# Kernel optimization log

Hardware: AMD Instinct MI355X
Metric: run time of the kernel (lower is better)

## Reference

```python
import jax, jax.numpy as jnp
import numpy as np

NEG_SLOPE = 0.2  # PyG GATConv default leaky_relu slope
EPS = 1e-16     # PyG softmax denominator epsilon


def gat_conv(x, src, dst, W, att_src, att_dst, bias, concat, num_nodes):
    """PyG-style GATConv (eval mode, dropout disabled).
    x: [N, F_in]; W: [F_in, H*C]; att_src/att_dst: [H, C]; bias: [H*C] or [C].
    Messages flow src -> dst; softmax is per destination node."""
    H, C = att_src.shape
    h = (x @ W).reshape(num_nodes, H, C)                      # [N,H,C]
    a_src = jnp.sum(h * att_src[None], axis=-1)               # [N,H]
    a_dst = jnp.sum(h * att_dst[None], axis=-1)               # [N,H]
    e = jax.nn.leaky_relu(a_src[src] + a_dst[dst], NEG_SLOPE) # [E,H]
    # numerically-stable segment softmax over edges grouped by dst
    m = jax.ops.segment_max(e, dst, num_segments=num_nodes)   # [N,H]
    ex = jnp.exp(e - m[dst])                                  # [E,H]
    s = jax.ops.segment_sum(ex, dst, num_segments=num_nodes)  # [N,H]
    alpha = ex / (s[dst] + EPS)                               # [E,H]
    msg = h[src] * alpha[..., None]                           # [E,H,C]
    out = jax.ops.segment_sum(msg, dst, num_segments=num_nodes)  # [N,H,C]
    if concat:
        out = out.reshape(num_nodes, H * C)
    else:
        out = out.mean(axis=1)                                # [N,C]
    return out + bias, alpha


def setup_inputs() -> dict:
    key = jax.random.key(0)
    ks = jax.random.split(key, 20)
    N, E = 50000, 500000
    F_node = 128       # num_node_features
    SED = 128          # sentence_embedding_dim
    HID = 64           # hidden_channels
    H = 2              # num_heads

    def g(k, shape, scale=0.05):
        return jax.random.normal(k, shape, dtype=jnp.float32) * scale

    return {
        "x": jax.random.normal(ks[0], (N, SED), dtype=jnp.float32),
        "edge_index": jax.random.randint(ks[1], (2, E), 0, N, dtype=jnp.int64),
        "cls_emb": jax.random.normal(ks[2], (768,), dtype=jnp.float32),
        # fc0: Linear(768, SED)
        "fc0_w": g(ks[3], (SED, 768)), "fc0_b": g(ks[4], (SED,)),
        # conv1: GATConv(2*SED -> HID, heads=H, concat=True)
        "W1": g(ks[5], (2 * SED, H * HID)),
        "att_src1": g(ks[6], (H, HID)), "att_dst1": g(ks[7], (H, HID)),
        "bias1": g(ks[8], (H * HID,)),
        # conv2: GATConv(H*HID -> F_node, heads=H, concat=False)
        "W2": g(ks[9], (H * HID, H * F_node)),
        "att_src2": g(ks[10], (H, F_node)), "att_dst2": g(ks[11], (H, F_node)),
        "bias2": g(ks[12], (F_node,)),
        # edge MLP head
        "fc2_w": g(ks[13], (F_node, 2 * F_node)), "fc2_b": g(ks[14], (F_node,)),
        "fc3_w": g(ks[15], (1, F_node)), "fc3_b": g(ks[16], (1,)),
    }


def reference(x, edge_index, cls_emb, fc0_w, fc0_b,
              W1, att_src1, att_dst1, bias1,
              W2, att_src2, att_dst2, bias2,
              fc2_w, fc2_b, fc3_w, fc3_b):
    N = x.shape[0]
    src, dst = edge_index[0], edge_index[1]
    # sentence embedding projection + broadcast-concat to every node
    sent = fc0_w @ cls_emb + fc0_b                                # [SED]
    h = jnp.concatenate([x, jnp.broadcast_to(sent, (N, sent.shape[0]))], axis=1)
    h, _ = gat_conv(h, src, dst, W1, att_src1, att_dst1, bias1, True, N)
    h = jax.nn.elu(h)
    h, _ = gat_conv(h, src, dst, W2, att_src2, att_dst2, bias2, False, N)
    # edge head: gather endpoints, concat, MLP, sigmoid
    edge_input = jnp.concatenate([h[src], h[dst]], axis=1)        # [E, 2*F]
    z = jax.nn.relu(edge_input @ fc2_w.T + fc2_b)                 # [E, F]
    logits = z @ fc3_w.T + fc3_b                                  # [E, 1]
    return jax.nn.sigmoid(logits)
```

## Files before the change

### kernel.cpp

```cpp
#include <hip/hip_runtime.h>
#include <hip/hip_bf16.h>
#include <math.h>


typedef short short8 __attribute__((ext_vector_type(8)));
typedef float floatx4 __attribute__((ext_vector_type(4)));
typedef float v2f __attribute__((ext_vector_type(2)));
typedef unsigned uint2v __attribute__((ext_vector_type(2)));

__device__ __forceinline__ v2f bfpair(unsigned v) {
    uint2v t; t.x = v << 16; t.y = v & 0xFFFF0000u;
    return __builtin_bit_cast(v2f, t);
}
__device__ __forceinline__ unsigned short bfbits(float f) {
    return __builtin_bit_cast(unsigned short, __float2bfloat16(f));
}
__device__ __forceinline__ unsigned packbf(float a, float b) {
    return ((unsigned)bfbits(b) << 16) | (unsigned)bfbits(a);
}
__device__ __forceinline__ float lrelu(float v) { return v > 0.f ? v : 0.2f * v; }

__global__ void prep_kernel(const float* __restrict__ cls, const float* __restrict__ fc0_w,
                            const float* __restrict__ fc0_b, const float* __restrict__ W1,
                            const float* __restrict__ W2, const float* __restrict__ fc2_w,
                            float* __restrict__ c1,
                            __hip_bfloat16* __restrict__ w1frag,
                            __hip_bfloat16* __restrict__ w2frag,
                            __hip_bfloat16* __restrict__ fc2frag,
                            int* __restrict__ counts, int N) {
    int tid = threadIdx.x;
    int gstride = gridDim.x * blockDim.x;
    int g = blockIdx.x * blockDim.x + tid;
    for (int i = g; i < N; i += gstride) counts[i] = 0;
    if (blockIdx.x == 0) {
        __shared__ float s_sent[128];
        if (tid < 128) {
            float acc = fc0_b[tid];
            const float* row = fc0_w + (size_t)tid * 768;
            for (int k = 0; k < 768; ++k) acc += row[k] * cls[k];
            s_sent[tid] = acc;
        }
        __syncthreads();
        if (tid < 128) {
            float acc = 0.f;
            for (int k = 0; k < 128; ++k) acc += s_sent[k] * W1[(128 + k) * 128 + tid];
            c1[tid] = acc;
        }
    }
    for (int i = g; i < 16384; i += gstride) {
        int j = i & 7, l = (i >> 3) & 63, nt = (i >> 9) & 7, kt = (i >> 12) & 3;
        int k = kt * 32 + (l >> 4) * 8 + j;
        int n = nt * 16 + (l & 15);
        w1frag[i] = __float2bfloat16(W1[k * 128 + n]);
    }
    for (int i = g; i < 32768; i += gstride) {
        int j = i & 7, l = (i >> 3) & 63, nt = (i >> 9) & 15, kt = (i >> 13) & 3;
        int k = kt * 32 + (l >> 4) * 8 + j;
        int n = nt * 16 + (l & 15);
        w2frag[i] = __float2bfloat16(W2[k * 256 + n]);
    }
    for (int i = g; i < 32768; i += gstride) {
        int j = i & 7, l = (i >> 3) & 63, nt = (i >> 9) & 15, kt = (i >> 13) & 3;
        int k = kt * 32 + (l >> 4) * 8 + j;
        int n = nt * 16 + (l & 15);
        float v = (n < 128) ? fc2_w[n * 256 + k] : fc2_w[(n - 128) * 256 + 128 + k];
        fc2frag[i] = __float2bfloat16(v);
    }
}

__global__ void __launch_bounds__(256) bsum_kernel(const int* __restrict__ counts,
                                                   int* __restrict__ bsum, int N) {
    int base = blockIdx.x * 1024;
    int tid = threadIdx.x;
    int v = 0;
    #pragma unroll
    for (int k = 0; k < 4; ++k) {
        int idx = base + k * 256 + tid;
        if (idx < N) v += counts[idx];
    }
    #pragma unroll
    for (int off = 1; off < 64; off <<= 1) v += __shfl_xor(v, off, 64);
    __shared__ int ws[4];
    if ((tid & 63) == 0) ws[tid >> 6] = v;
    __syncthreads();
    if (tid == 0) bsum[blockIdx.x] = ws[0] + ws[1] + ws[2] + ws[3];
}

__global__ void top_scan_kernel(const int* __restrict__ bsum, int* __restrict__ boff, int nb) {
    int lane = threadIdx.x;
    int v = (lane < nb) ? bsum[lane] : 0;
    int x = v;
    #pragma unroll
    for (int off = 1; off < 64; off <<= 1) {
        int t = __shfl_up(x, off, 64);
        if (lane >= off) x += t;
    }
    if (lane < nb) boff[lane] = x - v;
}

__global__ void __launch_bounds__(1024) local_scan_kernel(const int* __restrict__ counts,
                                                          const int* __restrict__ boff,
                                                          int* __restrict__ row, int* __restrict__ woff,
                                                          int N, int E) {
    int tid = threadIdx.x, lane = tid & 63, wv = tid >> 6;
    int base = blockIdx.x * 1024;
    __shared__ int wsum[16];
    int v = (base + tid < N) ? counts[base + tid] : 0;
    int x = v;
    #pragma unroll
    for (int off = 1; off < 64; off <<= 1) {
        int t = __shfl_up(x, off, 64);
        if (lane >= off) x += t;
    }
    if (lane == 63) wsum[wv] = x;
    __syncthreads();
    if (wv == 0 && lane < 16) {
        int y = wsum[lane];
        #pragma unroll
        for (int off = 1; off < 16; off <<= 1) {
            int t = __shfl_up(y, off, 64);
            if (lane >= off) y += t;
        }
        wsum[lane] = y;
    }
    __syncthreads();
    int excl = boff[blockIdx.x] + (wv ? wsum[wv - 1] : 0) + x - v;
    if (base + tid < N) { row[base + tid] = excl; woff[base + tid] = excl; }
    if (blockIdx.x == 0 && tid == 0) row[N] = E;
}

__global__ void scatter_kernel(const int* __restrict__ src, const int* __restrict__ dst,
                               int* __restrict__ woff, int* __restrict__ srcs, int E) {
    int e = blockIdx.x * blockDim.x + threadIdx.x;
    if (e < E) {
        int pos = atomicAdd(&woff[dst[e]], 1);
        srcs[pos] = src[e];
    }
}

__global__ void __launch_bounds__(256) gemm1_count_kernel(
        const float* __restrict__ x, const __hip_bfloat16* __restrict__ wfrag,
        const float* __restrict__ c1, const float* __restrict__ att_s, const float* __restrict__ att_d,
        __hip_bfloat16* __restrict__ h1bf, float* __restrict__ a_src, float* __restrict__ a_dst,
        const int* __restrict__ dst, int* __restrict__ counts, int E, int G1, int N) {
    if ((int)blockIdx.x >= G1) {
        int e = ((int)blockIdx.x - G1) * 256 + threadIdx.x;
        if (e < E) atomicAdd(&counts[dst[e]], 1);
        return;
    }
    int lane = threadIdx.x & 63, wv = threadIdx.x >> 6;
    int lo = lane & 15, quad = lane >> 4;
    int rowbase = ((int)blockIdx.x * 4 + wv) * 16;
    if (rowbase >= N) return;
    int arow = rowbase + lo; if (arow >= N) arow = N - 1;
    const float* ap = x + (size_t)arow * 128 + quad * 8;
    floatx4 acc[8];
    #pragma unroll
    for (int nt = 0; nt < 8; ++nt) acc[nt] = (floatx4){0.f, 0.f, 0.f, 0.f};
    const short8* bf = (const short8*)wfrag;
    #pragma unroll
    for (int kt = 0; kt < 4; ++kt) {
        float4 fa = *(const float4*)(ap + kt * 32);
        float4 fb = *(const float4*)(ap + kt * 32 + 4);
        short8 a;
        a[0] = (short)bfbits(fa.x); a[1] = (short)bfbits(fa.y);
        a[2] = (short)bfbits(fa.z); a[3] = (short)bfbits(fa.w);
        a[4] = (short)bfbits(fb.x); a[5] = (short)bfbits(fb.y);
        a[6] = (short)bfbits(fb.z); a[7] = (short)bfbits(fb.w);
        #pragma unroll
        for (int nt = 0; nt < 8; ++nt)
            acc[nt] = __builtin_amdgcn_mfma_f32_16x16x32_bf16(a, bf[(kt * 8 + nt) * 64 + lane], acc[nt], 0, 0, 0);
    }
    float ps0[4] = {0,0,0,0}, ps1[4] = {0,0,0,0}, pd0[4] = {0,0,0,0}, pd1[4] = {0,0,0,0};
    #pragma unroll
    for (int nt = 0; nt < 8; ++nt) {
        int ch = nt * 16 + lo;
        float cv = c1[ch], as_v = att_s[ch], ad_v = att_d[ch];
        #pragma unroll
        for (int r = 0; r < 4; ++r) {
            int row = rowbase + quad * 4 + r;
            float val = acc[nt][r] + cv;
            if (row < N) ((unsigned short*)h1bf)[(size_t)row * 128 + ch] = bfbits(val);
            if (nt < 4) { ps0[r] += val * as_v; pd0[r] += val * ad_v; }
            else        { ps1[r] += val * as_v; pd1[r] += val * ad_v; }
        }
    }
    #pragma unroll
    for (int r = 0; r < 4; ++r) {
        int row = rowbase + quad * 4 + r;
        float v0 = ps0[r], v1 = ps1[r], v2 = pd0[r], v3 = pd1[r];
        #pragma unroll
        for (int off = 1; off < 16; off <<= 1) {
            v0 += __shfl_xor(v0, off, 64); v1 += __shfl_xor(v1, off, 64);
            v2 += __shfl_xor(v2, off, 64); v3 += __shfl_xor(v3, off, 64);
        }
        if (lo == 0 && row < N) {
            a_src[row * 2 + 0] = v0; a_src[row * 2 + 1] = v1;
            a_dst[row * 2 + 0] = v2; a_dst[row * 2 + 1] = v3;
        }
    }
}

__global__ void __launch_bounds__(256) agg1_csr_kernel(
        const int* __restrict__ row, const int* __restrict__ srcs,
        const float* __restrict__ a_src, const float* __restrict__ a_dst,
        const unsigned* __restrict__ h1u, const float* __restrict__ bias1,
        unsigned* __restrict__ hmid_u, int N) {
    int tid = threadIdx.x;
    int d = blockIdx.x * 16 + (tid >> 4);
    if (d >= N) return;
    int q = tid & 15;
    int beg = row[d], end = row[d + 1];
    float2 adp = ((const float2*)a_dst)[d];
    float den0 = 0.f, den1 = 0.f;
    v2f facc2[4];
    #pragma unroll
    for (int m = 0; m < 4; ++m) facc2[m] = (v2f){0.f, 0.f};
    for (int i = beg; i < end; i += 4) {
        bool h1 = (i + 1) < end, h2 = (i + 2) < end, h3 = (i + 3) < end;
        int s0 = srcs[i];
        int s1 = h1 ? srcs[i + 1] : s0;
        int s2 = h2 ? srcs[i + 2] : s0;
        int s3 = h3 ? srcs[i + 3] : s0;
        float2 as0 = ((const float2*)a_src)[s0];
        float2 as1 = ((const float2*)a_src)[s1];
        float2 as2 = ((const float2*)a_src)[s2];
        float2 as3 = ((const float2*)a_src)[s3];
        uint4 u0 = ((const uint4*)(h1u + (size_t)s0 * 64))[q];
        uint4 u1 = ((const uint4*)(h1u + (size_t)s1 * 64))[q];
        uint4 u2 = ((const uint4*)(h1u + (size_t)s2 * 64))[q];
        uint4 u3 = ((const uint4*)(h1u + (size_t)s3 * 64))[q];
        float e00 = __expf(lrelu(as0.x + adp.x));
        float e01 = __expf(lrelu(as0.y + adp.y));
        float e10 = h1 ? __expf(lrelu(as1.x + adp.x)) : 0.f;
        float e11 = h1 ? __expf(lrelu(as1.y + adp.y)) : 0.f;
        float e20 = h2 ? __expf(lrelu(as2.x + adp.x)) : 0.f;
        float e21 = h2 ? __expf(lrelu(as2.y + adp.y)) : 0.f;
        float e30 = h3 ? __expf(lrelu(as3.x + adp.x)) : 0.f;
        float e31 = h3 ? __expf(lrelu(as3.y + adp.y)) : 0.f;
        den0 += e00 + e10 + e20 + e30;
        den1 += e01 + e11 + e21 + e31;
        float w0 = (q < 8) ? e00 : e01;
        float w1 = (q < 8) ? e10 : e11;
        float w2 = (q < 8) ? e20 : e21;
        float w3 = (q < 8) ? e30 : e31;
        facc2[0] += bfpair(u0.x) * w0 + bfpair(u1.x) * w1 + bfpair(u2.x) * w2 + bfpair(u3.x) * w3;
        facc2[1] += bfpair(u0.y) * w0 + bfpair(u1.y) * w1 + bfpair(u2.y) * w2 + bfpair(u3.y) * w3;
        facc2[2] += bfpair(u0.z) * w0 + bfpair(u1.z) * w1 + bfpair(u2.z) * w2 + bfpair(u3.z) * w3;
        facc2[3] += bfpair(u0.w) * w0 + bfpair(u1.w) * w1 + bfpair(u2.w) * w2 + bfpair(u3.w) * w3;
    }
    float inv = 1.f / (((q < 8) ? den0 : den1) + 1e-16f);
    int c0 = 8 * q;
    float v[8];
    #pragma unroll
    for (int m = 0; m < 4; ++m) {
        float va = facc2[m].x * inv + bias1[c0 + 2 * m];
        float vb = facc2[m].y * inv + bias1[c0 + 2 * m + 1];
        v[2 * m]     = va > 0.f ? va : expm1f(va);
        v[2 * m + 1] = vb > 0.f ? vb : expm1f(vb);
    }
    uint4 o;
    o.x = packbf(v[0], v[1]); o.y = packbf(v[2], v[3]);
    o.z = packbf(v[4], v[5]); o.w = packbf(v[6], v[7]);
    ((uint4*)(hmid_u + (size_t)d * 64))[q] = o;
}

__global__ void __launch_bounds__(256) gemm2_mfma_kernel(
        const __hip_bfloat16* __restrict__ hmid, const __hip_bfloat16* __restrict__ wfrag,
        const float* __restrict__ att_s, const float* __restrict__ att_d,
        __hip_bfloat16* __restrict__ h2pre, float* __restrict__ a_src, float* __restrict__ a_dst, int N) {
    int lane = threadIdx.x & 63, wv = threadIdx.x >> 6;
    int lo = lane & 15, quad = lane >> 4;
    int rowbase = (blockIdx.x * 4 + wv) * 16;
    if (rowbase >= N) return;
    int arow = rowbase + lo; if (arow >= N) arow = N - 1;
    const __hip_bfloat16* ap = hmid + (size_t)arow * 128 + quad * 8;
    floatx4 acc[16];
    #pragma unroll
    for (int nt = 0; nt < 16; ++nt) acc[nt] = (floatx4){0.f, 0.f, 0.f, 0.f};
    const short8* bf = (const short8*)wfrag;
    #pragma unroll
    for (int kt = 0; kt < 4; ++kt) {
        short8 a = *(const short8*)(ap + kt * 32);
        #pragma unroll
        for (int nt = 0; nt < 16; ++nt)
            acc[nt] = __builtin_amdgcn_mfma_f32_16x16x32_bf16(a, bf[(kt * 16 + nt) * 64 + lane], acc[nt], 0, 0, 0);
    }
    float ps0[4] = {0,0,0,0}, ps1[4] = {0,0,0,0}, pd0[4] = {0,0,0,0}, pd1[4] = {0,0,0,0};
    #pragma unroll
    for (int nt = 0; nt < 16; ++nt) {
        int ch = nt * 16 + lo;
        float as_v = att_s[ch], ad_v = att_d[ch];
        #pragma unroll
        for (int r = 0; r < 4; ++r) {
            int row = rowbase + quad * 4 + r;
            float val = acc[nt][r];
            if (row < N) ((unsigned short*)h2pre)[(size_t)row * 256 + ch] = bfbits(val);
            if (nt < 8) { ps0[r] += val * as_v; pd0[r] += val * ad_v; }
            else        { ps1[r] += val * as_v; pd1[r] += val * ad_v; }
        }
    }
    #pragma unroll
    for (int r = 0; r < 4; ++r) {
        int row = rowbase + quad * 4 + r;
        float v0 = ps0[r], v1 = ps1[r], v2 = pd0[r], v3 = pd1[r];
        #pragma unroll
        for (int off = 1; off < 16; off <<= 1) {
            v0 += __shfl_xor(v0, off, 64); v1 += __shfl_xor(v1, off, 64);
            v2 += __shfl_xor(v2, off, 64); v3 += __shfl_xor(v3, off, 64);
        }
        if (lo == 0 && row < N) {
            a_src[row * 2 + 0] = v0; a_src[row * 2 + 1] = v1;
            a_dst[row * 2 + 0] = v2; a_dst[row * 2 + 1] = v3;
        }
    }
}

__global__ void __launch_bounds__(256) agg2_csr_kernel(
        const int* __restrict__ row, const int* __restrict__ srcs,
        const float* __restrict__ a_src, const float* __restrict__ a_dst,
        const unsigned* __restrict__ h2u, const float* __restrict__ bias2,
        unsigned* __restrict__ h2bf_u, int N) {
    int tid = threadIdx.x;
    int d = blockIdx.x * 8 + (tid >> 5);
    if (d >= N) return;
    int q = tid & 31;
    int beg = row[d], end = row[d + 1];
    float2 adp = ((const float2*)a_dst)[d];
    float den0 = 0.f, den1 = 0.f;
    v2f facc2[4];
    #pragma unroll
    for (int m = 0; m < 4; ++m) facc2[m] = (v2f){0.f, 0.f};
    for (int i = beg; i < end; i += 4) {
        bool h1 = (i + 1) < end, h2 = (i + 2) < end, h3 = (i + 3) < end;
        int s0 = srcs[i];
        int s1 = h1 ? srcs[i + 1] : s0;
        int s2 = h2 ? srcs[i + 2] : s0;
        int s3 = h3 ? srcs[i + 3] : s0;
        float2 as0 = ((const float2*)a_src)[s0];
        float2 as1 = ((const float2*)a_src)[s1];
        float2 as2 = ((const float2*)a_src)[s2];
        float2 as3 = ((const float2*)a_src)[s3];
        uint4 u0 = ((const uint4*)(h2u + (size_t)s0 * 128))[q];
        uint4 u1 = ((const uint4*)(h2u + (size_t)s1 * 128))[q];
        uint4 u2 = ((const uint4*)(h2u + (size_t)s2 * 128))[q];
        uint4 u3 = ((const uint4*)(h2u + (size_t)s3 * 128))[q];
        float e00 = __expf(lrelu(as0.x + adp.x));
        float e01 = __expf(lrelu(as0.y + adp.y));
        float e10 = h1 ? __expf(lrelu(as1.x + adp.x)) : 0.f;
        float e11 = h1 ? __expf(lrelu(as1.y + adp.y)) : 0.f;
        float e20 = h2 ? __expf(lrelu(as2.x + adp.x)) : 0.f;
        float e21 = h2 ? __expf(lrelu(as2.y + adp.y)) : 0.f;
        float e30 = h3 ? __expf(lrelu(as3.x + adp.x)) : 0.f;
        float e31 = h3 ? __expf(lrelu(as3.y + adp.y)) : 0.f;
        den0 += e00 + e10 + e20 + e30;
        den1 += e01 + e11 + e21 + e31;
        float w0 = (q < 16) ? e00 : e01;
        float w1 = (q < 16) ? e10 : e11;
        float w2 = (q < 16) ? e20 : e21;
        float w3 = (q < 16) ? e30 : e31;
        facc2[0] += bfpair(u0.x) * w0 + bfpair(u1.x) * w1 + bfpair(u2.x) * w2 + bfpair(u3.x) * w3;
        facc2[1] += bfpair(u0.y) * w0 + bfpair(u1.y) * w1 + bfpair(u2.y) * w2 + bfpair(u3.y) * w3;
        facc2[2] += bfpair(u0.z) * w0 + bfpair(u1.z) * w1 + bfpair(u2.z) * w2 + bfpair(u3.z) * w3;
        facc2[3] += bfpair(u0.w) * w0 + bfpair(u1.w) * w1 + bfpair(u2.w) * w2 + bfpair(u3.w) * w3;
    }
    float inv = 0.5f / (((q < 16) ? den0 : den1) + 1e-16f);
    #pragma unroll
    for (int m = 0; m < 4; ++m) {
        facc2[m] *= inv;
        facc2[m].x += __shfl_xor(facc2[m].x, 16, 64);
        facc2[m].y += __shfl_xor(facc2[m].y, 16, 64);
    }
    if (q < 16) {
        int c0 = 8 * q;
        uint4 o;
        o.x = packbf(facc2[0].x + bias2[c0 + 0], facc2[0].y + bias2[c0 + 1]);
        o.y = packbf(facc2[1].x + bias2[c0 + 2], facc2[1].y + bias2[c0 + 3]);
        o.z = packbf(facc2[2].x + bias2[c0 + 4], facc2[2].y + bias2[c0 + 5]);
        o.w = packbf(facc2[3].x + bias2[c0 + 6], facc2[3].y + bias2[c0 + 7]);
        ((uint4*)(h2bf_u + (size_t)d * 64))[q] = o;
    }
}

__global__ void __launch_bounds__(256) zsd_mfma_kernel(
        const __hip_bfloat16* __restrict__ h2bf, const __hip_bfloat16* __restrict__ wfrag,
        const float* __restrict__ fc2_b, __hip_bfloat16* __restrict__ zsd, int N) {
    int lane = threadIdx.x & 63, wv = threadIdx.x >> 6;
    int lo = lane & 15, quad = lane >> 4;
    int rowbase = (blockIdx.x * 4 + wv) * 16;
    if (rowbase >= N) return;
    int arow = rowbase + lo; if (arow >= N) arow = N - 1;
    const __hip_bfloat16* ap = h2bf + (size_t)arow * 128 + quad * 8;
    floatx4 acc[16];
    #pragma unroll
    for (int nt = 0; nt < 16; ++nt) acc[nt] = (floatx4){0.f, 0.f, 0.f, 0.f};
    const short8* bf = (const short8*)wfrag;
    #pragma unroll
    for (int kt = 0; kt < 4; ++kt) {
        short8 a = *(const short8*)(ap + kt * 32);
        #pragma unroll
        for (int nt = 0; nt < 16; ++nt)
            acc[nt] = __builtin_amdgcn_mfma_f32_16x16x32_bf16(a, bf[(kt * 16 + nt) * 64 + lane], acc[nt], 0, 0, 0);
    }
    #pragma unroll
    for (int nt = 0; nt < 16; ++nt) {
        int ch = nt * 16 + lo;
        float bv = (nt >= 8) ? fc2_b[ch - 128] : 0.f;
        #pragma unroll
        for (int r = 0; r < 4; ++r) {
            int row = rowbase + quad * 4 + r;
            if (row < N) ((unsigned short*)zsd)[(size_t)row * 256 + ch] = bfbits(acc[nt][r] + bv);
        }
    }
}

__global__ void __launch_bounds__(256) edge_zsd_kernel(
        const int* __restrict__ src, const int* __restrict__ dst,
        const unsigned* __restrict__ zsd_u, const float* __restrict__ fc3_w,
        const float* __restrict__ fc3_b, float* __restrict__ out, int E) {
    int lane = threadIdx.x & 63, wv = threadIdx.x >> 6;
    int g = lane >> 5, r = (lane >> 4) & 1, q = lane & 15;
    int base = (blockIdx.x * 4 + wv) * 16;
    if (base >= E) return;
    v2f f30 = {fc3_w[8 * q + 4 * r + 0], fc3_w[8 * q + 4 * r + 1]};
    v2f f31 = {fc3_w[8 * q + 4 * r + 2], fc3_w[8 * q + 4 * r + 3]};
    float b3 = fc3_b[0];
    int nodes[8];
    #pragma unroll
    for (int j = 0; j < 8; ++j) {
        int e = base + 2 * j + g;
        int ec = e < E ? e : E - 1;
        nodes[j] = r ? dst[ec] : src[ec];
    }
    uint4 rows[8];
    #pragma unroll
    for (int j = 0; j < 8; ++j)
        rows[j] = ((const uint4*)(zsd_u + (size_t)nodes[j] * 128 + (r << 6)))[q];
    #pragma unroll
    for (int j = 0; j < 8; ++j) {
        uint4 mine = rows[j];
        unsigned sx = (unsigned)__shfl_xor((int)mine.x, 16, 64);
        unsigned sy = (unsigned)__shfl_xor((int)mine.y, 16, 64);
        unsigned sz = (unsigned)__shfl_xor((int)mine.z, 16, 64);
        unsigned sw = (unsigned)__shfl_xor((int)mine.w, 16, 64);
        unsigned mA = r ? mine.z : mine.x;
        unsigned mB = r ? mine.w : mine.y;
        unsigned oA = r ? sz : sx;
        unsigned oB = r ? sw : sy;
        v2f sA = bfpair(mA) + bfpair(oA);
        v2f sB = bfpair(mB) + bfpair(oB);
        sA.x = fmaxf(sA.x, 0.f); sA.y = fmaxf(sA.y, 0.f);
        sB.x = fmaxf(sB.x, 0.f); sB.y = fmaxf(sB.y, 0.f);
        v2f p2 = sA * f30 + sB * f31;
        float p = p2.x + p2.y;
        #pragma unroll
        for (int off = 1; off < 32; off <<= 1) p += __shfl_xor(p, off, 64);
        int e = base + 2 * j + g;
        if ((lane & 31) == 0 && e < E)
            out[e] = 1.f / (1.f + expf(-(p + b3)));
    }
}

extern "C" void kernel_launch(void* const* d_in, const int* in_sizes, int n_in,
                              void* d_out, int out_size, void* d_ws, size_t ws_size,
                              hipStream_t stream) {
    const float* x      = (const float*)d_in[0];
    const int*   ei     = (const int*)d_in[1];
    const float* cls    = (const float*)d_in[2];
    const float* fc0_w  = (const float*)d_in[3];
    const float* fc0_b  = (const float*)d_in[4];
    const float* W1     = (const float*)d_in[5];
    const float* att_s1 = (const float*)d_in[6];
    const float* att_d1 = (const float*)d_in[7];
    const float* bias1  = (const float*)d_in[8];
    const float* W2     = (const float*)d_in[9];
    const float* att_s2 = (const float*)d_in[10];
    const float* att_d2 = (const float*)d_in[11];
    const float* bias2  = (const float*)d_in[12];
    const float* fc2_w  = (const float*)d_in[13];
    const float* fc2_b  = (const float*)d_in[14];
    const float* fc3_w  = (const float*)d_in[15];
    const float* fc3_b  = (const float*)d_in[16];
    float* out = (float*)d_out;

    int N = in_sizes[0] / 128;
    int E = in_sizes[1] / 2;
    const int* src = ei;
    const int* dst = ei + E;
    int nb = (N + 1023) / 1024;

    float* w = (float*)d_ws;
    size_t off = 0;
    auto alloc = [&](size_t n) { float* p = w + off; off += (n + 63) & ~(size_t)63; return p; };
    float* c1      = alloc(128);
    float* w1fragf = alloc(16384 / 2);
    float* w2fragf = alloc(32768 / 2);
    float* fc2fragf= alloc(32768 / 2);
    float* a_s1    = alloc((size_t)N * 2);
    float* a_d1    = alloc((size_t)N * 2);
    float* a_s2    = alloc((size_t)N * 2);
    float* a_d2    = alloc((size_t)N * 2);
    float* h1bff   = alloc((size_t)N * 64);
    float* hmidf   = alloc((size_t)N * 64);
    float* h2pref  = alloc((size_t)N * 128);
    float* h2bff   = alloc((size_t)N * 64);
    float* zsdf    = alloc((size_t)N * 128);
    int* counts = (int*)alloc(N);
    int* rowp   = (int*)alloc(N + 1);
    int* woff   = (int*)alloc(N);
    int* srcs   = (int*)alloc(E);
    int* bsum   = (int*)alloc(64);
    int* boff   = (int*)alloc(64);
    __hip_bfloat16* w1frag = (__hip_bfloat16*)w1fragf;
    __hip_bfloat16* w2frag = (__hip_bfloat16*)w2fragf;
    __hip_bfloat16* fc2frag= (__hip_bfloat16*)fc2fragf;
    __hip_bfloat16* hmid   = (__hip_bfloat16*)hmidf;
    __hip_bfloat16* h2pre  = (__hip_bfloat16*)h2pref;
    __hip_bfloat16* h2bf   = (__hip_bfloat16*)h2bff;
    __hip_bfloat16* h1bf   = (__hip_bfloat16*)h1bff;
    __hip_bfloat16* zsd    = (__hip_bfloat16*)zsdf;

    prep_kernel<<<64, 256, 0, stream>>>(cls, fc0_w, fc0_b, W1, W2, fc2_w, c1, w1frag, w2frag, fc2frag,
                                        counts, N);
    int G1 = (N + 63) / 64;
    int G2 = (E + 255) / 256;
    gemm1_count_kernel<<<G1 + G2, 256, 0, stream>>>(x, w1frag, c1, att_s1, att_d1, h1bf, a_s1, a_d1,
                                                    dst, counts, E, G1, N);
    bsum_kernel<<<nb, 256, 0, stream>>>(counts, bsum, N);
    top_scan_kernel<<<1, 64, 0, stream>>>(bsum, boff, nb);
    local_scan_kernel<<<nb, 1024, 0, stream>>>(counts, boff, rowp, woff, N, E);
    scatter_kernel<<<(E + 255) / 256, 256, 0, stream>>>(src, dst, woff, srcs, E);
    agg1_csr_kernel<<<(N + 15) / 16, 256, 0, stream>>>(rowp, srcs, a_s1, a_d1, (const unsigned*)h1bf, bias1, (unsigned*)hmid, N);
    gemm2_mfma_kernel<<<(N + 63) / 64, 256, 0, stream>>>(hmid, w2frag, att_s2, att_d2, h2pre, a_s2, a_d2, N);
    agg2_csr_kernel<<<(N + 7) / 8, 256, 0, stream>>>(rowp, srcs, a_s2, a_d2, (const unsigned*)h2pre, bias2, (unsigned*)h2bf, N);
    zsd_mfma_kernel<<<(N + 63) / 64, 256, 0, stream>>>(h2bf, fc2frag, fc2_b, zsd, N);
    edge_zsd_kernel<<<(E + 63) / 64, 256, 0, stream>>>(src, dst, (const unsigned*)zsd, fc3_w, fc3_b, out, E);
}
```

Before: 329.4 us.

## Fold W2 into fc2 weights and aggregate layer-2 on 128-wide hmid

Uses linearity to reorder layer 2: the aggregation runs over the 128-channel hmid features per head instead of the 256-channel projected h2, and W2 is pre-multiplied into fc2 (with the head mean) as one 256x256 weight. The second-layer attention scores are computed in agg1's epilogue via precomputed W2·att vectors, which removes the gemm2 kernel and the h2pre round trip. The aggregation gather now reads half the bytes per edge. In exchange the zsd GEMM's K doubles to 256, and prep does a serial 128-length dot per weight element, about 65k of them.

```diff
diff --git a/kernel.cpp b/kernel.cpp
--- a/kernel.cpp
+++ b/kernel.cpp
@@ -23,10 +23,13 @@
 __global__ void prep_kernel(const float* __restrict__ cls, const float* __restrict__ fc0_w,
                             const float* __restrict__ fc0_b, const float* __restrict__ W1,
                             const float* __restrict__ W2, const float* __restrict__ fc2_w,
+                            const float* __restrict__ fc2_b, const float* __restrict__ bias2,
+                            const float* __restrict__ att_s2, const float* __restrict__ att_d2,
                             float* __restrict__ c1,
                             __hip_bfloat16* __restrict__ w1frag,
-                            __hip_bfloat16* __restrict__ w2frag,
-                            __hip_bfloat16* __restrict__ fc2frag,
+                            __hip_bfloat16* __restrict__ wbigfrag,
+                            float* __restrict__ v2s, float* __restrict__ v2d,
+                            float* __restrict__ bz,
                             int* __restrict__ counts, int N) {
     int tid = threadIdx.x;
     int gstride = gridDim.x * blockDim.x;
@@ -53,18 +56,34 @@
         int n = nt * 16 + (l & 15);
         w1frag[i] = __float2bfloat16(W1[k * 128 + n]);
     }
-    for (int i = g; i < 32768; i += gstride) {
-        int j = i & 7, l = (i >> 3) & 63, nt = (i >> 9) & 15, kt = (i >> 13) & 3;
+    for (int i = g; i < 65536; i += gstride) {
+        int j = i & 7, l = (i >> 3) & 63, nt = (i >> 9) & 15, kt = (i >> 13) & 7;
         int k = kt * 32 + (l >> 4) * 8 + j;
         int n = nt * 16 + (l & 15);
-        w2frag[i] = __float2bfloat16(W2[k * 256 + n]);
-    }
-    for (int i = g; i < 32768; i += gstride) {
-        int j = i & 7, l = (i >> 3) & 63, nt = (i >> 9) & 15, kt = (i >> 13) & 3;
-        int k = kt * 32 + (l >> 4) * 8 + j;
-        int n = nt * 16 + (l & 15);
-        float v = (n < 128) ? fc2_w[n * 256 + k] : fc2_w[(n - 128) * 256 + 128 + k];
-        fc2frag[i] = __float2bfloat16(v);
+        int h = k >> 7, kp = k & 127;
+        const float* w2row = W2 + (size_t)kp * 256 + h * 128;
+        const float* fcrow = (n < 128) ? (fc2_w + (size_t)n * 256)
+                                       : (fc2_w + (size_t)(n - 128) * 256 + 128);
+        float acc = 0.f;
+        for (int c2 = 0; c2 < 128; ++c2) acc += w2row[c2] * fcrow[c2];
+        wbigfrag[i] = __float2bfloat16(0.5f * acc);
+    }
+    for (int i = g; i < 256; i += gstride) {
+        int h = i >> 7, kp = i & 127;
+        const float* w2row = W2 + (size_t)kp * 256 + h * 128;
+        const float* as = att_s2 + h * 128;
+        const float* ad = att_d2 + h * 128;
+        float s = 0.f, dd = 0.f;
+        for (int c = 0; c < 128; ++c) { s += w2row[c] * as[c]; dd += w2row[c] * ad[c]; }
+        v2s[i] = s; v2d[i] = dd;
+    }
+    for (int i = g; i < 256; i += gstride) {
+        const float* fcrow = (i < 128) ? (fc2_w + (size_t)i * 256)
+                                       : (fc2_w + (size_t)(i - 128) * 256 + 128);
+        float acc = 0.f;
+        for (int c = 0; c < 128; ++c) acc += bias2[c] * fcrow[c];
+        if (i >= 128) acc += fc2_b[i - 128];
+        bz[i] = acc;
     }
 }
 
@@ -205,7 +224,8 @@
         const int* __restrict__ row, const int* __restrict__ srcs,
         const float* __restrict__ a_src, const float* __restrict__ a_dst,
         const unsigned* __restrict__ h1u, const float* __restrict__ bias1,
-        unsigned* __restrict__ hmid_u, int N) {
+        const float* __restrict__ v2s, const float* __restrict__ v2d,
+        unsigned* __restrict__ hmid_u, float* __restrict__ a_s2, float* __restrict__ a_d2, int N) {
     int tid = threadIdx.x;
     int d = blockIdx.x * 16 + (tid >> 4);
     if (d >= N) return;
@@ -263,74 +283,40 @@
     o.x = packbf(v[0], v[1]); o.y = packbf(v[2], v[3]);
     o.z = packbf(v[4], v[5]); o.w = packbf(v[6], v[7]);
     ((uint4*)(hmid_u + (size_t)d * 64))[q] = o;
-}
-
-__global__ void __launch_bounds__(256) gemm2_mfma_kernel(
-        const __hip_bfloat16* __restrict__ hmid, const __hip_bfloat16* __restrict__ wfrag,
-        const float* __restrict__ att_s, const float* __restrict__ att_d,
-        __hip_bfloat16* __restrict__ h2pre, float* __restrict__ a_src, float* __restrict__ a_dst, int N) {
-    int lane = threadIdx.x & 63, wv = threadIdx.x >> 6;
-    int lo = lane & 15, quad = lane >> 4;
-    int rowbase = (blockIdx.x * 4 + wv) * 16;
-    if (rowbase >= N) return;
-    int arow = rowbase + lo; if (arow >= N) arow = N - 1;
-    const __hip_bfloat16* ap = hmid + (size_t)arow * 128 + quad * 8;
-    floatx4 acc[16];
-    #pragma unroll
-    for (int nt = 0; nt < 16; ++nt) acc[nt] = (floatx4){0.f, 0.f, 0.f, 0.f};
-    const short8* bf = (const short8*)wfrag;
-    #pragma unroll
-    for (int kt = 0; kt < 4; ++kt) {
-        short8 a = *(const short8*)(ap + kt * 32);
-        #pragma unroll
-        for (int nt = 0; nt < 16; ++nt)
-            acc[nt] = __builtin_amdgcn_mfma_f32_16x16x32_bf16(a, bf[(kt * 16 + nt) * 64 + lane], acc[nt], 0, 0, 0);
-    }
-    float ps0[4] = {0,0,0,0}, ps1[4] = {0,0,0,0}, pd0[4] = {0,0,0,0}, pd1[4] = {0,0,0,0};
-    #pragma unroll
-    for (int nt = 0; nt < 16; ++nt) {
-        int ch = nt * 16 + lo;
-        float as_v = att_s[ch], ad_v = att_d[ch];
-        #pragma unroll
-        for (int r = 0; r < 4; ++r) {
-            int row = rowbase + quad * 4 + r;
-            float val = acc[nt][r];
-            if (row < N) ((unsigned short*)h2pre)[(size_t)row * 256 + ch] = bfbits(val);
-            if (nt < 8) { ps0[r] += val * as_v; pd0[r] += val * ad_v; }
-            else        { ps1[r] += val * as_v; pd1[r] += val * ad_v; }
-        }
-    }
-    #pragma unroll
-    for (int r = 0; r < 4; ++r) {
-        int row = rowbase + quad * 4 + r;
-        float v0 = ps0[r], v1 = ps1[r], v2 = pd0[r], v3 = pd1[r];
-        #pragma unroll
-        for (int off = 1; off < 16; off <<= 1) {
-            v0 += __shfl_xor(v0, off, 64); v1 += __shfl_xor(v1, off, 64);
-            v2 += __shfl_xor(v2, off, 64); v3 += __shfl_xor(v3, off, 64);
-        }
-        if (lo == 0 && row < N) {
-            a_src[row * 2 + 0] = v0; a_src[row * 2 + 1] = v1;
-            a_dst[row * 2 + 0] = v2; a_dst[row * 2 + 1] = v3;
-        }
-    }
-}
-
-__global__ void __launch_bounds__(256) agg2_csr_kernel(
+    float s20 = 0.f, s21 = 0.f, d20 = 0.f, d21 = 0.f;
+    #pragma unroll
+    for (int m = 0; m < 8; ++m) {
+        float hv = v[m];
+        s20 += hv * v2s[c0 + m];
+        s21 += hv * v2s[128 + c0 + m];
+        d20 += hv * v2d[c0 + m];
+        d21 += hv * v2d[128 + c0 + m];
+    }
+    #pragma unroll
+    for (int off = 1; off < 16; off <<= 1) {
+        s20 += __shfl_xor(s20, off, 64); s21 += __shfl_xor(s21, off, 64);
+        d20 += __shfl_xor(d20, off, 64); d21 += __shfl_xor(d21, off, 64);
+    }
+    if (q == 0) {
+        ((float2*)a_s2)[d] = make_float2(s20, s21);
+        ((float2*)a_d2)[d] = make_float2(d20, d21);
+    }
+}
+
+__global__ void __launch_bounds__(256) agg2m_csr_kernel(
         const int* __restrict__ row, const int* __restrict__ srcs,
         const float* __restrict__ a_src, const float* __restrict__ a_dst,
-        const unsigned* __restrict__ h2u, const float* __restrict__ bias2,
-        unsigned* __restrict__ h2bf_u, int N) {
+        const unsigned* __restrict__ hmid_u, unsigned* __restrict__ Acat_u, int N) {
     int tid = threadIdx.x;
-    int d = blockIdx.x * 8 + (tid >> 5);
+    int d = blockIdx.x * 16 + (tid >> 4);
     if (d >= N) return;
-    int q = tid & 31;
+    int q = tid & 15;
     int beg = row[d], end = row[d + 1];
     float2 adp = ((const float2*)a_dst)[d];
     float den0 = 0.f, den1 = 0.f;
-    v2f facc2[4];
-    #pragma unroll
-    for (int m = 0; m < 4; ++m) facc2[m] = (v2f){0.f, 0.f};
+    v2f a0[4], a1[4];
+    #pragma unroll
+    for (int m = 0; m < 4; ++m) { a0[m] = (v2f){0.f, 0.f}; a1[m] = (v2f){0.f, 0.f}; }
     for (int i = beg; i < end; i += 4) {
         bool h1 = (i + 1) < end, h2 = (i + 2) < end, h3 = (i + 3) < end;
         int s0 = srcs[i];
@@ -341,10 +327,10 @@
         float2 as1 = ((const float2*)a_src)[s1];
         float2 as2 = ((const float2*)a_src)[s2];
         float2 as3 = ((const float2*)a_src)[s3];
-        uint4 u0 = ((const uint4*)(h2u + (size_t)s0 * 128))[q];
-        uint4 u1 = ((const uint4*)(h2u + (size_t)s1 * 128))[q];
-        uint4 u2 = ((const uint4*)(h2u + (size_t)s2 * 128))[q];
-        uint4 u3 = ((const uint4*)(h2u + (size_t)s3 * 128))[q];
+        uint4 u0 = ((const uint4*)(hmid_u + (size_t)s0 * 64))[q];
+        uint4 u1 = ((const uint4*)(hmid_u + (size_t)s1 * 64))[q];
+        uint4 u2 = ((const uint4*)(hmid_u + (size_t)s2 * 64))[q];
+        uint4 u3 = ((const uint4*)(hmid_u + (size_t)s3 * 64))[q];
         float e00 = __expf(lrelu(as0.x + adp.x));
         float e01 = __expf(lrelu(as0.y + adp.y));
         float e10 = h1 ? __expf(lrelu(as1.x + adp.x)) : 0.f;
@@ -355,48 +341,50 @@
         float e31 = h3 ? __expf(lrelu(as3.y + adp.y)) : 0.f;
         den0 += e00 + e10 + e20 + e30;
         den1 += e01 + e11 + e21 + e31;
-        float w0 = (q < 16) ? e00 : e01;
-        float w1 = (q < 16) ? e10 : e11;
-        float w2 = (q < 16) ? e20 : e21;
-        float w3 = (q < 16) ? e30 : e31;
-        facc2[0] += bfpair(u0.x) * w0 + bfpair(u1.x) * w1 + bfpair(u2.x) * w2 + bfpair(u3.x) * w3;
-        facc2[1] += bfpair(u0.y) * w0 + bfpair(u1.y) * w1 + bfpair(u2.y) * w2 + bfpair(u3.y) * w3;
-        facc2[2] += bfpair(u0.z) * w0 + bfpair(u1.z) * w1 + bfpair(u2.z) * w2 + bfpair(u3.z) * w3;
-        facc2[3] += bfpair(u0.w) * w0 + bfpair(u1.w) * w1 + bfpair(u2.w) * w2 + bfpair(u3.w) * w3;
-    }
-    float inv = 0.5f / (((q < 16) ? den0 : den1) + 1e-16f);
-    #pragma unroll
-    for (int m = 0; m < 4; ++m) {
-        facc2[m] *= inv;
-        facc2[m].x += __shfl_xor(facc2[m].x, 16, 64);
-        facc2[m].y += __shfl_xor(facc2[m].y, 16, 64);
-    }
-    if (q < 16) {
-        int c0 = 8 * q;
-        uint4 o;
-        o.x = packbf(facc2[0].x + bias2[c0 + 0], facc2[0].y + bias2[c0 + 1]);
-        o.y = packbf(facc2[1].x + bias2[c0 + 2], facc2[1].y + bias2[c0 + 3]);
-        o.z = packbf(facc2[2].x + bias2[c0 + 4], facc2[2].y + bias2[c0 + 5]);
-        o.w = packbf(facc2[3].x + bias2[c0 + 6], facc2[3].y + bias2[c0 + 7]);
-        ((uint4*)(h2bf_u + (size_t)d * 64))[q] = o;
-    }
+        v2f p0x = bfpair(u0.x), p0y = bfpair(u0.y), p0z = bfpair(u0.z), p0w = bfpair(u0.w);
+        v2f p1x = bfpair(u1.x), p1y = bfpair(u1.y), p1z = bfpair(u1.z), p1w = bfpair(u1.w);
+        v2f p2x = bfpair(u2.x), p2y = bfpair(u2.y), p2z = bfpair(u2.z), p2w = bfpair(u2.w);
+        v2f p3x = bfpair(u3.x), p3y = bfpair(u3.y), p3z = bfpair(u3.z), p3w = bfpair(u3.w);
+        a0[0] += p0x * e00 + p1x * e10 + p2x * e20 + p3x * e30;
+        a0[1] += p0y * e00 + p1y * e10 + p2y * e20 + p3y * e30;
+        a0[2] += p0z * e00 + p1z * e10 + p2z * e20 + p3z * e30;
+        a0[3] += p0w * e00 + p1w * e10 + p2w * e20 + p3w * e30;
+        a1[0] += p0x * e01 + p1x * e11 + p2x * e21 + p3x * e31;
+        a1[1] += p0y * e01 + p1y * e11 + p2y * e21 + p3y * e31;
+        a1[2] += p0z * e01 + p1z * e11 + p2z * e21 + p3z * e31;
+        a1[3] += p0w * e01 + p1w * e11 + p2w * e21 + p3w * e31;
+    }
+    float inv0 = 1.f / (den0 + 1e-16f);
+    float inv1 = 1.f / (den1 + 1e-16f);
+    uint4 o0, o1;
+    o0.x = packbf(a0[0].x * inv0, a0[0].y * inv0);
+    o0.y = packbf(a0[1].x * inv0, a0[1].y * inv0);
+    o0.z = packbf(a0[2].x * inv0, a0[2].y * inv0);
+    o0.w = packbf(a0[3].x * inv0, a0[3].y * inv0);
+    o1.x = packbf(a1[0].x * inv1, a1[0].y * inv1);
+    o1.y = packbf(a1[1].x * inv1, a1[1].y * inv1);
+    o1.z = packbf(a1[2].x * inv1, a1[2].y * inv1);
+    o1.w = packbf(a1[3].x * inv1, a1[3].y * inv1);
+    uint4* orow = (uint4*)(Acat_u + (size_t)d * 128);
+    orow[q] = o0;
+    orow[16 + q] = o1;
 }
 
 __global__ void __launch_bounds__(256) zsd_mfma_kernel(
-        const __hip_bfloat16* __restrict__ h2bf, const __hip_bfloat16* __restrict__ wfrag,
-        const float* __restrict__ fc2_b, __hip_bfloat16* __restrict__ zsd, int N) {
+        const __hip_bfloat16* __restrict__ Acat, const __hip_bfloat16* __restrict__ wfrag,
+        const float* __restrict__ bz, __hip_bfloat16* __restrict__ zsd, int N) {
     int lane = threadIdx.x & 63, wv = threadIdx.x >> 6;
     int lo = lane & 15, quad = lane >> 4;
     int rowbase = (blockIdx.x * 4 + wv) * 16;
     if (rowbase >= N) return;
     int arow = rowbase + lo; if (arow >= N) arow = N - 1;
-    const __hip_bfloat16* ap = h2bf + (size_t)arow * 128 + quad * 8;
+    const __hip_bfloat16* ap = Acat + (size_t)arow * 256 + quad * 8;
     floatx4 acc[16];
     #pragma unroll
     for (int nt = 0; nt < 16; ++nt) acc[nt] = (floatx4){0.f, 0.f, 0.f, 0.f};
     const short8* bf = (const short8*)wfrag;
     #pragma unroll
-    for (int kt = 0; kt < 4; ++kt) {
+    for (int kt = 0; kt < 8; ++kt) {
         short8 a = *(const short8*)(ap + kt * 32);
         #pragma unroll
         for (int nt = 0; nt < 16; ++nt)
@@ -405,7 +393,7 @@
     #pragma unroll
     for (int nt = 0; nt < 16; ++nt) {
         int ch = nt * 16 + lo;
-        float bv = (nt >= 8) ? fc2_b[ch - 128] : 0.f;
+        float bv = bz[ch];
         #pragma unroll
         for (int r = 0; r < 4; ++r) {
             int row = rowbase + quad * 4 + r;
@@ -492,35 +480,35 @@
     float* w = (float*)d_ws;
     size_t off = 0;
     auto alloc = [&](size_t n) { float* p = w + off; off += (n + 63) & ~(size_t)63; return p; };
-    float* c1      = alloc(128);
-    float* w1fragf = alloc(16384 / 2);
-    float* w2fragf = alloc(32768 / 2);
-    float* fc2fragf= alloc(32768 / 2);
-    float* a_s1    = alloc((size_t)N * 2);
-    float* a_d1    = alloc((size_t)N * 2);
-    float* a_s2    = alloc((size_t)N * 2);
-    float* a_d2    = alloc((size_t)N * 2);
-    float* h1bff   = alloc((size_t)N * 64);
-    float* hmidf   = alloc((size_t)N * 64);
-    float* h2pref  = alloc((size_t)N * 128);
-    float* h2bff   = alloc((size_t)N * 64);
-    float* zsdf    = alloc((size_t)N * 128);
+    float* c1       = alloc(128);
+    float* w1fragf  = alloc(16384 / 2);
+    float* wbigf    = alloc(65536 / 2);
+    float* v2s      = alloc(256);
+    float* v2d      = alloc(256);
+    float* bz       = alloc(256);
+    float* a_s1     = alloc((size_t)N * 2);
+    float* a_d1     = alloc((size_t)N * 2);
+    float* a_s2     = alloc((size_t)N * 2);
+    float* a_d2     = alloc((size_t)N * 2);
+    float* h1bff    = alloc((size_t)N * 64);
+    float* hmidf    = alloc((size_t)N * 64);
+    float* Acatf    = alloc((size_t)N * 128);
+    float* zsdf     = alloc((size_t)N * 128);
     int* counts = (int*)alloc(N);
     int* rowp   = (int*)alloc(N + 1);
     int* woff   = (int*)alloc(N);
     int* srcs   = (int*)alloc(E);
     int* bsum   = (int*)alloc(64);
     int* boff   = (int*)alloc(64);
-    __hip_bfloat16* w1frag = (__hip_bfloat16*)w1fragf;
-    __hip_bfloat16* w2frag = (__hip_bfloat16*)w2fragf;
-    __hip_bfloat16* fc2frag= (__hip_bfloat16*)fc2fragf;
-    __hip_bfloat16* hmid   = (__hip_bfloat16*)hmidf;
-    __hip_bfloat16* h2pre  = (__hip_bfloat16*)h2pref;
-    __hip_bfloat16* h2bf   = (__hip_bfloat16*)h2bff;
-    __hip_bfloat16* h1bf   = (__hip_bfloat16*)h1bff;
-    __hip_bfloat16* zsd    = (__hip_bfloat16*)zsdf;
-
-    prep_kernel<<<64, 256, 0, stream>>>(cls, fc0_w, fc0_b, W1, W2, fc2_w, c1, w1frag, w2frag, fc2frag,
+    __hip_bfloat16* w1frag   = (__hip_bfloat16*)w1fragf;
+    __hip_bfloat16* wbigfrag = (__hip_bfloat16*)wbigf;
+    __hip_bfloat16* h1bf     = (__hip_bfloat16*)h1bff;
+    __hip_bfloat16* hmid     = (__hip_bfloat16*)hmidf;
+    __hip_bfloat16* Acat     = (__hip_bfloat16*)Acatf;
+    __hip_bfloat16* zsd      = (__hip_bfloat16*)zsdf;
+
+    prep_kernel<<<64, 256, 0, stream>>>(cls, fc0_w, fc0_b, W1, W2, fc2_w, fc2_b, bias2,
+                                        att_s2, att_d2, c1, w1frag, wbigfrag, v2s, v2d, bz,
                                         counts, N);
     int G1 = (N + 63) / 64;
     int G2 = (E + 255) / 256;
@@ -530,9 +518,10 @@
     top_scan_kernel<<<1, 64, 0, stream>>>(bsum, boff, nb);
     local_scan_kernel<<<nb, 1024, 0, stream>>>(counts, boff, rowp, woff, N, E);
     scatter_kernel<<<(E + 255) / 256, 256, 0, stream>>>(src, dst, woff, srcs, E);
-    agg1_csr_kernel<<<(N + 15) / 16, 256, 0, stream>>>(rowp, srcs, a_s1, a_d1, (const unsigned*)h1bf, bias1, (unsigned*)hmid, N);
-    gemm2_mfma_kernel<<<(N + 63) / 64, 256, 0, stream>>>(hmid, w2frag, att_s2, att_d2, h2pre, a_s2, a_d2, N);
-    agg2_csr_kernel<<<(N + 7) / 8, 256, 0, stream>>>(rowp, srcs, a_s2, a_d2, (const unsigned*)h2pre, bias2, (unsigned*)h2bf, N);
-    zsd_mfma_kernel<<<(N + 63) / 64, 256, 0, stream>>>(h2bf, fc2frag, fc2_b, zsd, N);
+    agg1_csr_kernel<<<(N + 15) / 16, 256, 0, stream>>>(rowp, srcs, a_s1, a_d1, (const unsigned*)h1bf,
+                                                       bias1, v2s, v2d, (unsigned*)hmid, a_s2, a_d2, N);
+    agg2m_csr_kernel<<<(N + 15) / 16, 256, 0, stream>>>(rowp, srcs, a_s2, a_d2, (const unsigned*)hmid,
+                                                        (unsigned*)Acat, N);
+    zsd_mfma_kernel<<<(N + 63) / 64, 256, 0, stream>>>(Acat, wbigfrag, bz, zsd, N);
     edge_zsd_kernel<<<(E + 63) / 64, 256, 0, stream>>>(src, dst, (const unsigned*)zsd, fc3_w, fc3_b, out, E);
 }
```

Measured after the change: 340.3 us. 1.03x slower.
